# Optimization experiments

Hardware: AMD Instinct MI355X
Metric: run time of the kernel (lower is better)

## Reference

```python
import jax, jax.numpy as jnp
import numpy as np

N = 128          # seed length cfg.n
EXTRA_RANDOM = 1 # cfg.extra_random_masks


def _make_masks(n: int, extra: int) -> np.ndarray:
    i = np.arange(n, dtype=np.int64)
    # Thue-Morse: parity of popcount(i)
    tm = np.array([bin(v).count('1') & 1 for v in i], dtype=np.uint8)
    # Sierpinski: row (n-1) of Pascal's triangle mod 2 (Lucas' theorem)
    sp = (((n - 1) & i) == i).astype(np.uint8)
    masks = [sp, tm]
    rng = np.random.default_rng(1234)
    for _ in range(extra):
        masks.append(rng.integers(0, 2, size=n, dtype=np.uint8))
    return np.stack(masks, axis=0)  # (K, n)


def setup_inputs() -> dict:
    key = jax.random.key(0)
    ks = jax.random.split(key, 8)
    B, n = 64, N
    T = n * (n + 1) // 2  # 8256
    H = 1024
    x = jax.random.randint(ks[0], (B, n), 0, 2, dtype=jnp.int32)
    masks = jnp.asarray(_make_masks(n, EXTRA_RANDOM))
    def lin(k, fan_in, fan_out):
        lim = 1.0 / np.sqrt(fan_in)
        return jax.random.uniform(k, (fan_in, fan_out), jnp.float32, -lim, lim)
    W0 = lin(ks[1], T, H); b0 = jnp.zeros((H,), jnp.float32)
    W1 = lin(ks[2], H, H); b1 = jnp.zeros((H,), jnp.float32)
    Wo = lin(ks[3], H, 1); bo = jnp.zeros((1,), jnp.float32)
    return {"x": x, "masks": masks, "W0": W0, "b0": b0,
            "W1": W1, "b1": b1, "Wo": Wo, "bo": bo}


def _features(x, masks):
    # x: (B, n) ints in {0,1}; masks: (K, n) uint8
    xb = x.astype(jnp.uint8)
    B, n = xb.shape
    # L3: dihedral orbit = n rotations + n rotations of the reversal -> 2n seeds
    idx = (jnp.arange(n)[:, None] + jnp.arange(n)[None, :]) % n  # (n, n)
    rot = xb[:, idx]                # (B, n, n)
    rev = xb[:, ::-1][:, idx]       # (B, n, n)
    seeds = jnp.concatenate([rot, rev], axis=1)  # (B, 2n, n)
    # L4: keep each seed plus XOR with each mask -> (1+K) variants per seed
    masked = jnp.bitwise_xor(seeds[:, :, None, :], masks[None, None, :, :])  # (B,2n,K,n)
    all_seeds = jnp.concatenate([seeds[:, :, None, :], masked], axis=2)
    M = all_seeds.shape[1] * all_seeds.shape[2]
    all_seeds = all_seeds.reshape(B, M, n)  # (B, M, n) uint8
    # XNOR triangle: row0 = seed, row_{k+1}[j] = xnor(row_k[j], row_k[j+1])
    rows = [all_seeds]
    cur = all_seeds
    for _ in range(n - 1):
        cur = 1 - jnp.bitwise_xor(cur[..., :-1], cur[..., 1:])
        rows.append(cur)
    feats = jnp.concatenate(rows, axis=-1)          # (B, M, T(n)) uint8
    f = jnp.mean(feats, axis=1, dtype=jnp.float32)  # mean pool over transforms
    return 2.0 * f - 1.0                            # {0,1} -> {-1,+1}


def reference(x, masks, W0, b0, W1, b1, Wo, bo):
    f = _features(x, masks)
    h = jax.nn.relu(f @ W0 + b0)
    h = jax.nn.relu(h @ W1 + b1)
    return h @ Wo + bo  # (B, 1) logits
```

## Files before the change

### kernel.cpp

```cpp
#include <hip/hip_runtime.h>
#include <cstdint>

#define DEVFN __device__ __forceinline__

struct U128 { unsigned long long lo, hi; };

DEVFN U128 rotr128(U128 w, int s) {
    U128 r;
    if (s == 64) { r.lo = w.hi; r.hi = w.lo; return r; }
    if (s < 64) {
        r.lo = (w.lo >> s) | (w.hi << (64 - s));
        r.hi = (w.hi >> s) | (w.lo << (64 - s));
    } else {
        int t = s - 64;
        unsigned long long lo = w.hi, hi = w.lo;
        r.lo = (lo >> t) | (hi << (64 - t));
        r.hi = (hi >> t) | (lo << (64 - t));
    }
    return r;
}

DEVFN U128 shr128(U128 w, int s) {
    U128 r;
    if (s == 64) { r.lo = w.hi; r.hi = 0ull; return r; }
    if (s < 64) {
        r.lo = (w.lo >> s) | (w.hi << (64 - s));
        r.hi = w.hi >> s;
    } else {
        r.lo = w.hi >> (s - 64); r.hi = 0ull;
    }
    return r;
}

__global__ __launch_bounds__(256) void kB(const int* __restrict__ x,
                                          const int* __restrict__ masks,
                                          const float* __restrict__ W0,
                                          float* __restrict__ S,
                                          float* __restrict__ A2,
                                          float* __restrict__ G2) {
    int bid = blockIdx.x;
    int tid = threadIdx.x;

    if (bid == 768) {
        int b = tid >> 2;
        int rc = tid & 3;
        const int* xb = x + b * 128;
        U128 w; w.lo = 0ull; w.hi = 0ull;
        #pragma unroll
        for (int p = 0; p < 64; ++p) w.lo |= (unsigned long long)(xb[p] & 1) << p;
        #pragma unroll
        for (int p = 0; p < 64; ++p) w.hi |= (unsigned long long)(xb[64 + p] & 1) << p;
        int r0 = rc * 32;
        if (r0 & 32) { U128 t = rotr128(w, 32); w.lo ^= t.lo; w.hi ^= t.hi; }
        if (r0 & 64) { U128 t = rotr128(w, 64); w.lo ^= t.lo; w.hi ^= t.hi; }
        for (int rr = 0; rr < 32; ++rr) {
            int r = r0 + rr;
            int pc = __popcll(w.lo) + __popcll(w.hi);
            int sv = (r == 0) ? pc : (128 - pc);
            S[b * 128 + r] = (float)(2 * sv);
            U128 t = rotr128(w, 1);
            w.lo ^= t.lo; w.hi ^= t.hi;
        }
        return;
    }

    int hc = bid & 3;
    int y  = bid >> 2;
    int r, jstart, jend, slice;
    if (y < 128) { r = y >> 1; slice = y & 1; jstart = slice * 64; jend = (slice == 0) ? 64 : (128 - r); }
    else         { r = y - 64;  slice = 0;    jstart = 0;          jend = 128 - r; }

    int h = hc * 256 + tid;

    __shared__ unsigned long long mw[3][2];
    __shared__ float cA[64], cG[64];

    if (tid < 128) {
        int half = tid >> 6;
        int lane = tid & 63;
        #pragma unroll
        for (int k = 0; k < 3; ++k) {
            unsigned long long bal = __ballot(masks[k * 128 + half * 64 + lane] & 1);
            if (lane == 0) mw[k][half] = bal;
        }
    }
    __syncthreads();
    if (tid < 64) {
        int j = jstart + tid;
        int c = 0;
        #pragma unroll
        for (int k = 0; k < 3; ++k) {
            U128 m; m.lo = mw[k][0]; m.hi = mw[k][1];
            #pragma unroll
            for (int s = 1; s <= 64; s <<= 1) {
                if (r & s) { U128 t = shr128(m, s); m.lo ^= t.lo; m.hi ^= t.hi; }
            }
            int bit = (j < 64) ? (int)((m.lo >> j) & 1) : (int)((m.hi >> (j - 64)) & 1);
            c += bit;
        }
        cA[tid] = 0.5f * (float)c - 1.0f;
        cG[tid] = (float)(2 - c) * (1.0f / 256.0f);
    }
    __syncthreads();

    int off = r * 128 - (r * (r - 1)) / 2;
    const float* p = W0 + (off + jstart) * 1024 + h;
    int L = jend - jstart;
    float accA = 0.f, accG = 0.f;
    #pragma unroll 8
    for (int j = 0; j < L; ++j) {
        float w = p[j * 1024];
        accA += cA[j] * w;
        accG += cG[j] * w;
    }
    int row = slice * 128 + r;
    A2[row * 1024 + h] = accA;
    G2[row * 1024 + h] = accG;
}

__global__ __launch_bounds__(256) void kC(const float* __restrict__ A2,
                                          const float* __restrict__ G2,
                                          const float* __restrict__ S,
                                          const float* __restrict__ b0,
                                          float* __restrict__ h0) {
    int b  = blockIdx.x;
    int ht = blockIdx.y;
    int tid = threadIdx.x;
    int h = ht * 256 + tid;
    __shared__ float Srow[128];
    if (tid < 128) Srow[tid] = S[b * 128 + tid];
    __syncthreads();
    float acc = b0[h];
    #pragma unroll 8
    for (int r = 0; r < 64; ++r) {
        float a = A2[r * 1024 + h] + A2[(128 + r) * 1024 + h];
        float g = G2[r * 1024 + h] + G2[(128 + r) * 1024 + h];
        acc += a + Srow[r] * g;
    }
    #pragma unroll 8
    for (int r = 64; r < 128; ++r) {
        acc += A2[r * 1024 + h] + Srow[r] * G2[r * 1024 + h];
    }
    h0[b * 1024 + h] = fmaxf(acc, 0.f);
}

__global__ __launch_bounds__(256) void kD(const float* __restrict__ h0,
                                          const float* __restrict__ W1,
                                          float* __restrict__ z1part) {
    int hc = blockIdx.x;
    int kc = blockIdx.y;
    int tid = threadIdx.x;
    __shared__ float Wt[64][64];
    __shared__ float Ht[64][64];
    #pragma unroll
    for (int i = 0; i < 16; ++i) {
        int idx = tid + i * 256;
        int a = idx >> 6, c = idx & 63;
        Wt[a][c] = W1[(kc * 64 + a) * 1024 + hc * 64 + c];
        Ht[a][c] = h0[a * 1024 + kc * 64 + c];
    }
    __syncthreads();
    int h = tid & 63, bg = tid >> 6;
    float acc[16];
    #pragma unroll
    for (int i = 0; i < 16; ++i) acc[i] = 0.f;
    for (int k = 0; k < 64; k += 4) {
        float w0_ = Wt[k][h], w1_ = Wt[k + 1][h], w2_ = Wt[k + 2][h], w3_ = Wt[k + 3][h];
        #pragma unroll
        for (int bb = 0; bb < 16; ++bb) {
            float4 hv = *(const float4*)&Ht[bg * 16 + bb][k];
            acc[bb] += hv.x * w0_ + hv.y * w1_ + hv.z * w2_ + hv.w * w3_;
        }
    }
    #pragma unroll
    for (int bb = 0; bb < 16; ++bb) {
        int b = bg * 16 + bb;
        z1part[(kc * 64 + b) * 1024 + hc * 64 + h] = acc[bb];
    }
}

__global__ __launch_bounds__(256) void kE(const float* __restrict__ z1part,
                                          const float* __restrict__ b1,
                                          const float* __restrict__ Wo,
                                          const float* __restrict__ bo,
                                          float* __restrict__ out) {
    int b = blockIdx.x;
    int tid = threadIdx.x;
    float acc = 0.f;
    #pragma unroll
    for (int i = 0; i < 4; ++i) {
        int h = tid + i * 256;
        float z = b1[h];
        #pragma unroll
        for (int kc = 0; kc < 16; ++kc) z += z1part[(kc * 64 + b) * 1024 + h];
        acc += fmaxf(z, 0.f) * Wo[h];
    }
    #pragma unroll
    for (int off = 32; off >= 1; off >>= 1) acc += __shfl_down(acc, off);
    __shared__ float red[4];
    if ((tid & 63) == 0) red[tid >> 6] = acc;
    __syncthreads();
    if (tid == 0) out[b] = red[0] + red[1] + red[2] + red[3] + bo[0];
}

extern "C" void kernel_launch(void* const* d_in, const int* in_sizes, int n_in,
                              void* d_out, int out_size, void* d_ws, size_t ws_size,
                              hipStream_t stream) {
    const int*   x     = (const int*)d_in[0];
    const int*   masks = (const int*)d_in[1];
    const float* W0    = (const float*)d_in[2];
    const float* b0    = (const float*)d_in[3];
    const float* W1    = (const float*)d_in[4];
    const float* b1    = (const float*)d_in[5];
    const float* Wo    = (const float*)d_in[6];
    const float* bo    = (const float*)d_in[7];
    float* out = (float*)d_out;

    char* ws = (char*)d_ws;
    float* S      = (float*)(ws);
    float* A2     = (float*)(ws + (32u   << 10));
    float* G2     = (float*)(ws + (800u  << 10));
    float* h0     = (float*)(ws + (1568u << 10));
    float* z1part = (float*)(ws + (1824u << 10));

    kB<<<769, 256, 0, stream>>>(x, masks, W0, S, A2, G2);
    kC<<<dim3(64, 4), 256, 0, stream>>>(A2, G2, S, b0, h0);
    kD<<<dim3(16, 16), 256, 0, stream>>>(h0, W1, z1part);
    kE<<<64, 256, 0, stream>>>(z1part, b1, Wo, bo, out);
}
```

Baseline: 39.01 us.

## Repartition W0 reduction into 32-row chunks with float4 loads covering full H

The first kernel now splits each triangle row of W0 into chunks of up to 32 columns, giving 320 blocks. Each thread handles four hidden units through float4 loads, so every block covers all 1024 outputs. The aim is better load balance, fewer redundant mask/coefficient setups, and wider memory transactions on the dominant W0 stream. The h0 kernel is restructured to sum 320 partial rows via a lookup table mapping chunk to row, with 8 batch rows per block. The price is more partial-sum traffic and reads, and fewer blocks on a 256-CU part.

```diff
diff --git a/kernel.cpp b/kernel.cpp
--- a/kernel.cpp
+++ b/kernel.cpp
@@ -32,16 +32,19 @@
     return r;
 }
 
-__global__ __launch_bounds__(256) void kB(const int* __restrict__ x,
-                                          const int* __restrict__ masks,
-                                          const float* __restrict__ W0,
-                                          float* __restrict__ S,
-                                          float* __restrict__ A2,
-                                          float* __restrict__ G2) {
+DEVFN int fcum(int L) { int q = L >> 5, s = L & 31; return 16 * q * (q + 1) + s * (q + 1); }
+DEVFN int tstart(int r) { return 320 - fcum(128 - r); }
+
+__global__ __launch_bounds__(256) void k1_reduce(const int* __restrict__ x,
+                                                 const int* __restrict__ masks,
+                                                 const float* __restrict__ W0,
+                                                 float* __restrict__ S,
+                                                 float* __restrict__ A2,
+                                                 float* __restrict__ G2) {
     int bid = blockIdx.x;
     int tid = threadIdx.x;
 
-    if (bid == 768) {
+    if (bid == 320) {
         int b = tid >> 2;
         int rc = tid & 3;
         const int* xb = x + b * 128;
@@ -51,33 +54,31 @@
         #pragma unroll
         for (int p = 0; p < 64; ++p) w.hi |= (unsigned long long)(xb[64 + p] & 1) << p;
         int r0 = rc * 32;
-        if (r0 & 32) { U128 t = rotr128(w, 32); w.lo ^= t.lo; w.hi ^= t.hi; }
-        if (r0 & 64) { U128 t = rotr128(w, 64); w.lo ^= t.lo; w.hi ^= t.hi; }
+        if (r0 & 32) { U128 tt = rotr128(w, 32); w.lo ^= tt.lo; w.hi ^= tt.hi; }
+        if (r0 & 64) { U128 tt = rotr128(w, 64); w.lo ^= tt.lo; w.hi ^= tt.hi; }
         for (int rr = 0; rr < 32; ++rr) {
             int r = r0 + rr;
             int pc = __popcll(w.lo) + __popcll(w.hi);
             int sv = (r == 0) ? pc : (128 - pc);
             S[b * 128 + r] = (float)(2 * sv);
-            U128 t = rotr128(w, 1);
-            w.lo ^= t.lo; w.hi ^= t.hi;
+            U128 tt = rotr128(w, 1);
+            w.lo ^= tt.lo; w.hi ^= tt.hi;
         }
         return;
     }
 
-    int hc = bid & 3;
-    int y  = bid >> 2;
-    int r, jstart, jend, slice;
-    if (y < 128) { r = y >> 1; slice = y & 1; jstart = slice * 64; jend = (slice == 0) ? 64 : (128 - r); }
-    else         { r = y - 64;  slice = 0;    jstart = 0;          jend = 128 - r; }
-
-    int h = hc * 256 + tid;
+    int lo = 0, hi = 127;
+    while (lo < hi) { int mid = (lo + hi + 1) >> 1; if (tstart(mid) <= bid) lo = mid; else hi = mid - 1; }
+    int r = lo;
+    int c = bid - tstart(r);
+    int j0 = c * 32;
+    int L = 128 - r - j0; if (L > 32) L = 32;
 
     __shared__ unsigned long long mw[3][2];
-    __shared__ float cA[64], cG[64];
+    __shared__ float cA[32], cG[32];
 
     if (tid < 128) {
-        int half = tid >> 6;
-        int lane = tid & 63;
+        int half = tid >> 6, lane = tid & 63;
         #pragma unroll
         for (int k = 0; k < 3; ++k) {
             unsigned long long bal = __ballot(masks[k * 128 + half * 64 + lane] & 1);
@@ -85,68 +86,80 @@
         }
     }
     __syncthreads();
-    if (tid < 64) {
-        int j = jstart + tid;
-        int c = 0;
+    if (tid < 32) {
+        int j = j0 + tid;
+        int cc = 0;
         #pragma unroll
         for (int k = 0; k < 3; ++k) {
             U128 m; m.lo = mw[k][0]; m.hi = mw[k][1];
             #pragma unroll
             for (int s = 1; s <= 64; s <<= 1) {
-                if (r & s) { U128 t = shr128(m, s); m.lo ^= t.lo; m.hi ^= t.hi; }
+                if (r & s) { U128 tt = shr128(m, s); m.lo ^= tt.lo; m.hi ^= tt.hi; }
             }
             int bit = (j < 64) ? (int)((m.lo >> j) & 1) : (int)((m.hi >> (j - 64)) & 1);
-            c += bit;
-        }
-        cA[tid] = 0.5f * (float)c - 1.0f;
-        cG[tid] = (float)(2 - c) * (1.0f / 256.0f);
-    }
-    __syncthreads();
-
-    int off = r * 128 - (r * (r - 1)) / 2;
-    const float* p = W0 + (off + jstart) * 1024 + h;
-    int L = jend - jstart;
-    float accA = 0.f, accG = 0.f;
-    #pragma unroll 8
-    for (int j = 0; j < L; ++j) {
-        float w = p[j * 1024];
-        accA += cA[j] * w;
-        accG += cG[j] * w;
-    }
-    int row = slice * 128 + r;
-    A2[row * 1024 + h] = accA;
-    G2[row * 1024 + h] = accG;
-}
-
-__global__ __launch_bounds__(256) void kC(const float* __restrict__ A2,
-                                          const float* __restrict__ G2,
-                                          const float* __restrict__ S,
-                                          const float* __restrict__ b0,
-                                          float* __restrict__ h0) {
-    int b  = blockIdx.x;
-    int ht = blockIdx.y;
-    int tid = threadIdx.x;
-    int h = ht * 256 + tid;
-    __shared__ float Srow[128];
-    if (tid < 128) Srow[tid] = S[b * 128 + tid];
-    __syncthreads();
+            cc += bit;
+        }
+        cA[tid] = 0.5f * (float)cc - 1.0f;
+        cG[tid] = (float)(2 - cc) * (1.0f / 256.0f);
+    }
+    __syncthreads();
+
+    int rowoff = r * 128 - (r * (r - 1)) / 2 + j0;
+    const float4* p = (const float4*)(W0 + (size_t)rowoff * 1024) + tid;
+    float4 aA = {0.f, 0.f, 0.f, 0.f}, aG = {0.f, 0.f, 0.f, 0.f};
+    #pragma unroll 4
+    for (int jj = 0; jj < L; ++jj) {
+        float4 v = p[jj * 256];
+        float ca = cA[jj], cg = cG[jj];
+        aA.x += ca * v.x; aA.y += ca * v.y; aA.z += ca * v.z; aA.w += ca * v.w;
+        aG.x += cg * v.x; aG.y += cg * v.y; aG.z += cg * v.z; aG.w += cg * v.w;
+    }
+    ((float4*)(A2 + (size_t)bid * 1024))[tid] = aA;
+    ((float4*)(G2 + (size_t)bid * 1024))[tid] = aG;
+}
+
+__global__ __launch_bounds__(256) void k2_h0(const float* __restrict__ A2,
+                                             const float* __restrict__ G2,
+                                             const float* __restrict__ S,
+                                             const float* __restrict__ b0,
+                                             float* __restrict__ h0) {
+    int hc = blockIdx.x;
+    int bt = blockIdx.y;
+    int tid = threadIdx.x;
+    int hl = tid & 31, bl = tid >> 5;
+    int h = hc * 32 + hl;
+    int b = bt * 8 + bl;
+
+    __shared__ float Sblk[8][128];
+    __shared__ int   rtab[320];
+
+    #pragma unroll
+    for (int i = 0; i < 4; ++i) {
+        int idx = tid + i * 256;
+        int bb = idx >> 7, rr = idx & 127;
+        Sblk[bb][rr] = S[(bt * 8 + bb) * 128 + rr];
+    }
+    if (tid < 128) {
+        int r = tid;
+        int s0 = tstart(r);
+        int n = (128 - r + 31) >> 5;
+        for (int c = 0; c < n; ++c) rtab[s0 + c] = r;
+    }
+    __syncthreads();
+
     float acc = b0[h];
     #pragma unroll 8
-    for (int r = 0; r < 64; ++r) {
-        float a = A2[r * 1024 + h] + A2[(128 + r) * 1024 + h];
-        float g = G2[r * 1024 + h] + G2[(128 + r) * 1024 + h];
-        acc += a + Srow[r] * g;
-    }
-    #pragma unroll 8
-    for (int r = 64; r < 128; ++r) {
-        acc += A2[r * 1024 + h] + Srow[r] * G2[r * 1024 + h];
+    for (int row = 0; row < 320; ++row) {
+        float a = A2[row * 1024 + h];
+        float g = G2[row * 1024 + h];
+        acc += a + Sblk[bl][rtab[row]] * g;
     }
     h0[b * 1024 + h] = fmaxf(acc, 0.f);
 }
 
-__global__ __launch_bounds__(256) void kD(const float* __restrict__ h0,
-                                          const float* __restrict__ W1,
-                                          float* __restrict__ z1part) {
+__global__ __launch_bounds__(256) void k3_layer2(const float* __restrict__ h0,
+                                                 const float* __restrict__ W1,
+                                                 float* __restrict__ z1part) {
     int hc = blockIdx.x;
     int kc = blockIdx.y;
     int tid = threadIdx.x;
@@ -179,11 +192,11 @@
     }
 }
 
-__global__ __launch_bounds__(256) void kE(const float* __restrict__ z1part,
-                                          const float* __restrict__ b1,
-                                          const float* __restrict__ Wo,
-                                          const float* __restrict__ bo,
-                                          float* __restrict__ out) {
+__global__ __launch_bounds__(256) void k4_out(const float* __restrict__ z1part,
+                                              const float* __restrict__ b1,
+                                              const float* __restrict__ Wo,
+                                              const float* __restrict__ bo,
+                                              float* __restrict__ out) {
     int b = blockIdx.x;
     int tid = threadIdx.x;
     float acc = 0.f;
@@ -219,12 +232,12 @@
     char* ws = (char*)d_ws;
     float* S      = (float*)(ws);
     float* A2     = (float*)(ws + (32u   << 10));
-    float* G2     = (float*)(ws + (800u  << 10));
-    float* h0     = (float*)(ws + (1568u << 10));
-    float* z1part = (float*)(ws + (1824u << 10));
-
-    kB<<<769, 256, 0, stream>>>(x, masks, W0, S, A2, G2);
-    kC<<<dim3(64, 4), 256, 0, stream>>>(A2, G2, S, b0, h0);
-    kD<<<dim3(16, 16), 256, 0, stream>>>(h0, W1, z1part);
-    kE<<<64, 256, 0, stream>>>(z1part, b1, Wo, bo, out);
-}
+    float* G2     = (float*)(ws + (1312u << 10));
+    float* h0     = (float*)(ws + (2592u << 10));
+    float* z1part = (float*)(ws + (2848u << 10));
+
+    k1_reduce<<<321, 256, 0, stream>>>(x, masks, W0, S, A2, G2);
+    k2_h0<<<dim3(32, 8), 256, 0, stream>>>(A2, G2, S, b0, h0);
+    k3_layer2<<<dim3(16, 16), 256, 0, stream>>>(h0, W1, z1part);
+    k4_out<<<64, 256, 0, stream>>>(z1part, b1, Wo, bo, out);
+}
```

After: 46.16 us. +18.3%, slower.

## Reuse A2/G2 loads across multiple batch rows in kC

Applied to the files above, without the earlier changes.

Restructures kC so each block covers 64 hidden units and 16 batch rows, with each thread holding 4 batch accumulators. Each A2/G2 element is now loaded once per 16 batches instead of once per batch, which cuts redundant global reads. The batch-independent A sum is computed once per thread. The grid shrinks from 256 to 64 blocks, so parallelism is lower and latency hiding may suffer.

```diff
diff --git a/kernel.cpp b/kernel.cpp
--- a/kernel.cpp
+++ b/kernel.cpp
@@ -123,25 +123,40 @@
                                           const float* __restrict__ S,
                                           const float* __restrict__ b0,
                                           float* __restrict__ h0) {
-    int b  = blockIdx.x;
-    int ht = blockIdx.y;
-    int tid = threadIdx.x;
-    int h = ht * 256 + tid;
-    __shared__ float Srow[128];
-    if (tid < 128) Srow[tid] = S[b * 128 + tid];
-    __syncthreads();
-    float acc = b0[h];
-    #pragma unroll 8
-    for (int r = 0; r < 64; ++r) {
-        float a = A2[r * 1024 + h] + A2[(128 + r) * 1024 + h];
-        float g = G2[r * 1024 + h] + G2[(128 + r) * 1024 + h];
-        acc += a + Srow[r] * g;
-    }
-    #pragma unroll 8
-    for (int r = 64; r < 128; ++r) {
-        acc += A2[r * 1024 + h] + Srow[r] * G2[r * 1024 + h];
-    }
-    h0[b * 1024 + h] = fmaxf(acc, 0.f);
+    int hc = blockIdx.x;
+    int bt = blockIdx.y;
+    int tid = threadIdx.x;
+    int hl = tid & 63, bg = tid >> 6;
+    int h = hc * 64 + hl;
+
+    __shared__ float Ssh[128][16];
+    #pragma unroll
+    for (int i = 0; i < 8; ++i) {
+        int idx = tid + i * 256;
+        int r = idx >> 4, bl = idx & 15;
+        Ssh[r][bl] = S[(bt * 16 + bl) * 128 + r];
+    }
+    __syncthreads();
+
+    float accA = 0.f;
+    float acc[4] = {0.f, 0.f, 0.f, 0.f};
+    #pragma unroll 4
+    for (int row = 0; row < 192; ++row) {
+        int r = row & 127;
+        float a = A2[row * 1024 + h];
+        float g = G2[row * 1024 + h];
+        accA += a;
+        #pragma unroll
+        for (int bb = 0; bb < 4; ++bb) {
+            acc[bb] += Ssh[r][bg * 4 + bb] * g;
+        }
+    }
+    float base = b0[h] + accA;
+    #pragma unroll
+    for (int bb = 0; bb < 4; ++bb) {
+        int b = bt * 16 + bg * 4 + bb;
+        h0[b * 1024 + h] = fmaxf(base + acc[bb], 0.f);
+    }
 }
 
 __global__ __launch_bounds__(256) void kD(const float* __restrict__ h0,
@@ -224,7 +239,7 @@
     float* z1part = (float*)(ws + (1824u << 10));
 
     kB<<<769, 256, 0, stream>>>(x, masks, W0, S, A2, G2);
-    kC<<<dim3(64, 4), 256, 0, stream>>>(A2, G2, S, b0, h0);
+    kC<<<dim3(16, 4), 256, 0, stream>>>(A2, G2, S, b0, h0);
     kD<<<dim3(16, 16), 256, 0, stream>>>(h0, W1, z1part);
     kE<<<64, 256, 0, stream>>>(z1part, b1, Wo, bo, out);
 }
```

Result: slower. 50.51 us (+29.5%).
